# Performance work log

Measured on AMD Instinct MI355X. Metric: run time of the kernel, lower is better.

Reference implementation:

```python
import jax, jax.numpy as jnp
from jax import lax
import numpy as np

B = 4096          # batch
EMBED = 32        # embed_dim
HEADS = 2
MEM_SIZE = 4096
MEM_DIM = 256
TOPK = 10
LN_EPS = 1e-5


def setup_inputs() -> dict:
    key = jax.random.key(0)
    ks = jax.random.split(key, 32)
    rn = lambda i, shape, s=0.05: (jax.random.normal(ks[i], shape) * s).astype(jnp.float32)
    return {
        'x': jax.random.normal(ks[0], (B, 1, 28, 28), dtype=jnp.float32),
        'patch_w': rn(1, (32, 1, 4, 4)), 'patch_b': rn(2, (32,)),
        'blk_ln1_g': jnp.ones((2, 32), jnp.float32), 'blk_ln1_b': jnp.zeros((2, 32), jnp.float32),
        'blk_inproj_w': rn(3, (2, 96, 32)), 'blk_inproj_b': rn(4, (2, 96)),
        'blk_outproj_w': rn(5, (2, 32, 32)), 'blk_outproj_b': rn(6, (2, 32)),
        'blk_ln2_g': jnp.ones((2, 32), jnp.float32), 'blk_ln2_b': jnp.zeros((2, 32), jnp.float32),
        'blk_ff1_w': rn(7, (2, 128, 32)), 'blk_ff1_b': rn(8, (2, 128)),
        'blk_ff2_w': rn(9, (2, 32, 128)), 'blk_ff2_b': rn(10, (2, 32)),
        'lat_w': rn(11, (256, 1568)), 'lat_b': rn(12, (256,)),
        'memory': jax.random.normal(ks[13], (MEM_SIZE, MEM_DIM), dtype=jnp.float32),
        'dec_w': rn(14, (3136, 256)), 'dec_b': rn(15, (3136,)),
        'upt1_w': rn(16, (64, 32, 4, 4)), 'upt1_b': rn(17, (32,)),
        'c1_w': rn(18, (32, 32, 3, 3)), 'c1_b': rn(19, (32,)),
        'upt2_w': rn(20, (32, 16, 4, 4)), 'upt2_b': rn(21, (16,)),
        'c2_w': rn(22, (8, 16, 3, 3)), 'c2_b': rn(23, (8,)),
        'c3_w': rn(24, (1, 8, 1, 1)), 'c3_b': rn(25, (1,)),
    }


def _ln(x, g, b):
    m = jnp.mean(x, -1, keepdims=True)
    v = jnp.mean((x - m) ** 2, -1, keepdims=True)
    return (x - m) / jnp.sqrt(v + LN_EPS) * g + b


def _conv2d(x, w, b, stride=1, pad=0):
    out = lax.conv_general_dilated(x, w, (stride, stride), ((pad, pad), (pad, pad)),
                                   dimension_numbers=('NCHW', 'OIHW', 'NCHW'))
    return out + b[None, :, None, None]


def _conv_transpose2d(x, w, b, stride, pad):
    # w in torch layout [in, out, kh, kw]; equivalent fractionally-strided conv
    w_f = jnp.flip(w, (2, 3)).transpose(1, 0, 2, 3)  # OIHW
    k = w.shape[2]
    p = k - 1 - pad
    out = lax.conv_general_dilated(x, w_f, (1, 1), ((p, p), (p, p)),
                                   lhs_dilation=(stride, stride),
                                   dimension_numbers=('NCHW', 'OIHW', 'NCHW'))
    return out + b[None, :, None, None]


def _mha(x, wi, bi, wo, bo):
    Bn, S, D = x.shape
    Dh = D // HEADS
    qkv = x @ wi.T + bi                                  # [B,S,3D]
    q, k, v = jnp.split(qkv, 3, axis=-1)
    sp = lambda t: t.reshape(Bn, S, HEADS, Dh).transpose(0, 2, 1, 3)
    q, k, v = sp(q), sp(k), sp(v)
    scores = jnp.einsum('bhqd,bhkd->bhqk', q, k) / jnp.sqrt(jnp.asarray(Dh, x.dtype))
    att = jax.nn.softmax(scores, axis=-1)
    o = jnp.einsum('bhqk,bhkd->bhqd', att, v).transpose(0, 2, 1, 3).reshape(Bn, S, D)
    return o @ wo.T + bo


def _memory_read(latent, memory):
    # cosine-sim topk softmax-weighted gather (F.normalize eps=1e-12)
    mn = memory / jnp.clip(jnp.linalg.norm(memory, axis=1, keepdims=True), 1e-12)
    xn = latent / jnp.clip(jnp.linalg.norm(latent, axis=1, keepdims=True), 1e-12)
    sim = xn @ mn.T                                       # [B, MEM_SIZE]
    topk_sim, topk_idx = lax.top_k(sim, TOPK)
    w = jax.nn.softmax(topk_sim, axis=1)                  # [B, TOPK]
    sel = memory[topk_idx]                                # [B, TOPK, MEM_DIM]
    return jnp.einsum('bk,bkd->bd', w, sel)


def _forward(x, patch_w, patch_b, blk_ln1_g, blk_ln1_b, blk_inproj_w, blk_inproj_b,
             blk_outproj_w, blk_outproj_b, blk_ln2_g, blk_ln2_b, blk_ff1_w, blk_ff1_b,
             blk_ff2_w, blk_ff2_b, lat_w, lat_b, memory, dec_w, dec_b,
             upt1_w, upt1_b, c1_w, c1_b, upt2_w, upt2_b, c2_w, c2_b, c3_w, c3_b):
    Bn = x.shape[0]
    h = _conv2d(x, patch_w, patch_b, stride=4)            # [B,32,7,7]
    t = h.reshape(Bn, EMBED, 49).transpose(0, 2, 1)       # [B,49,32]
    for i in range(2):                                    # two SwinBlocks
        t = t + _mha(_ln(t, blk_ln1_g[i], blk_ln1_b[i]),
                     blk_inproj_w[i], blk_inproj_b[i], blk_outproj_w[i], blk_outproj_b[i])
        f = _ln(t, blk_ln2_g[i], blk_ln2_b[i])
        f = jax.nn.gelu(f @ blk_ff1_w[i].T + blk_ff1_b[i], approximate=False)
        t = t + (f @ blk_ff2_w[i].T + blk_ff2_b[i])
    latent = t.reshape(Bn, -1) @ lat_w.T + lat_b          # [B,256]
    mem_latent = _memory_read(latent, memory)             # [B,256]
    d = (mem_latent @ dec_w.T + dec_b).reshape(Bn, 64, 7, 7)  # dropout=eval identity
    d = jax.nn.relu(_conv_transpose2d(d, upt1_w, upt1_b, 2, 1))   # [B,32,14,14]
    d = jax.nn.relu(_conv2d(d, c1_w, c1_b, 1, 1))
    d = jax.nn.relu(_conv_transpose2d(d, upt2_w, upt2_b, 2, 1))   # [B,16,28,28]
    d = jax.nn.relu(_conv2d(d, c2_w, c2_b, 1, 1))                 # [B,8,28,28]
    return _conv2d(d, c3_w, c3_b, 1, 0)                           # [B,1,28,28]


def reference(x, patch_w, patch_b, blk_ln1_g, blk_ln1_b, blk_inproj_w, blk_inproj_b,
              blk_outproj_w, blk_outproj_b, blk_ln2_g, blk_ln2_b, blk_ff1_w, blk_ff1_b,
              blk_ff2_w, blk_ff2_b, lat_w, lat_b, memory, dec_w, dec_b,
              upt1_w, upt1_b, c1_w, c1_b, upt2_w, upt2_b, c2_w, c2_b, c3_w, c3_b):
    return _forward(x, patch_w, patch_b, blk_ln1_g, blk_ln1_b, blk_inproj_w, blk_inproj_b,
                    blk_outproj_w, blk_outproj_b, blk_ln2_g, blk_ln2_b, blk_ff1_w, blk_ff1_b,
                    blk_ff2_w, blk_ff2_b, lat_w, lat_b, memory, dec_w, dec_b,
                    upt1_w, upt1_b, c1_w, c1_b, upt2_w, upt2_b, c2_w, c2_b, c3_w, c3_b)
```

## Files before the change

kernel.cpp:

```cpp
#include <hip/hip_runtime.h>
#include <math.h>

#define B_TOT 4096
#define CHUNK 4096

typedef _Float16 half_t;
typedef _Float16 h2 __attribute__((ext_vector_type(2)));
typedef _Float16 h8v __attribute__((ext_vector_type(8)));
typedef float f4v __attribute__((ext_vector_type(4)));

#if __has_builtin(__builtin_amdgcn_fdot2)
#define FDOT2(a, b, c) __builtin_amdgcn_fdot2((a), (b), (c), false)
#else
#define FDOT2(a, b, c) fmaf((float)(a)[1], (float)(b)[1], fmaf((float)(a)[0], (float)(b)[0], (c)))
#endif

#define KSTR 36
#define VSTR 34
#define KBYTES (49 * 72)
#define WAVE_LDS (49 * 72 + 49 * 136)
#define WI_OFF  (4 * WAVE_LDS)
#define BLOCK_LDS (WI_OFF + 12288)

__global__ __launch_bounds__(256) void k_tokens(
    const float* __restrict__ x, const float* __restrict__ pw, const float* __restrict__ pb,
    const float* __restrict__ ln1g, const float* __restrict__ ln1b,
    const float* __restrict__ wi, const float* __restrict__ bi,
    const float* __restrict__ wo, const float* __restrict__ bo,
    const float* __restrict__ ln2g, const float* __restrict__ ln2b,
    const float* __restrict__ w1, const float* __restrict__ fb1,
    const float* __restrict__ w2t, const float* __restrict__ fb2,
    float* __restrict__ tokens)
{
    __shared__ __align__(16) unsigned char Lraw[BLOCK_LDS];
    const int tid = threadIdx.x;
    const int wv = tid >> 6, lane = tid & 63;
    const int b = blockIdx.x * 4 + wv;
    half_t* Kb = (half_t*)(Lraw + wv * WAVE_LDS);
    float*  Vb = (float*)(Lraw + wv * WAVE_LDS + KBYTES);
    const float* wiL = (const float*)(Lraw + WI_OFF);
    float* Lf = (float*)Lraw;
    const bool is_tok = lane < 49;
    const int s = is_tok ? lane : 48;
    const int py = s / 7, px = s % 7;

    {
        const float4* srcw = (const float4*)(wi);
        float4* dstw = (float4*)(Lraw + WI_OFF);
        for (int e = tid; e < 768; e += 256) dstw[e] = srcw[e];
    }

    float xv[16];
    const float* xb = x + (size_t)b * 784 + py * 112 + px * 4;
    #pragma unroll
    for (int r = 0; r < 4; ++r) {
        float4 vq = *(const float4*)(xb + r * 28);
        xv[4 * r + 0] = vq.x; xv[4 * r + 1] = vq.y;
        xv[4 * r + 2] = vq.z; xv[4 * r + 3] = vq.w;
    }
    float t[32];
    #pragma unroll 4
    for (int c = 0; c < 32; ++c) {
        float a = pb[c];
        const float* wr = pw + c * 16;
        #pragma unroll
        for (int i = 0; i < 16; ++i) a = fmaf(xv[i], wr[i], a);
        t[c] = a;
    }

    for (int blk = 0; blk < 2; ++blk) {
        const float* bib = bi + blk * 96;

        float mu = 0.f;
        #pragma unroll
        for (int c = 0; c < 32; ++c) mu += t[c];
        mu *= 0.03125f;
        float var = 0.f;
        #pragma unroll
        for (int c = 0; c < 32; ++c) { float d = t[c] - mu; var = fmaf(d, d, var); }
        float rstd = rsqrtf(var * 0.03125f + 1e-5f);
        float xn[32];
        #pragma unroll
        for (int c = 0; c < 32; ++c)
            xn[c] = (t[c] - mu) * rstd * ln1g[blk * 32 + c] + ln1b[blk * 32 + c];

        __syncthreads();

        #pragma unroll 4
        for (int d = 0; d < 32; ++d) {
            const float* wr = wiL + (32 + d) * 32;
            float a0 = bib[32 + d], a1 = 0.f;
            #pragma unroll
            for (int c2 = 0; c2 < 4; ++c2) {
                float4 wq = *(const float4*)&wr[4 * c2];
                a0 = fmaf(xn[4 * c2],     wq.x, a0);
                a0 = fmaf(xn[4 * c2 + 1], wq.y, a0);
                a0 = fmaf(xn[4 * c2 + 2], wq.z, a0);
                a0 = fmaf(xn[4 * c2 + 3], wq.w, a0);
            }
            #pragma unroll
            for (int c2 = 4; c2 < 8; ++c2) {
                float4 wq = *(const float4*)&wr[4 * c2];
                a1 = fmaf(xn[4 * c2],     wq.x, a1);
                a1 = fmaf(xn[4 * c2 + 1], wq.y, a1);
                a1 = fmaf(xn[4 * c2 + 2], wq.z, a1);
                a1 = fmaf(xn[4 * c2 + 3], wq.w, a1);
            }
            if (is_tok) Kb[s * KSTR + d] = (half_t)(a0 + a1);
        }
        #pragma unroll 4
        for (int d = 0; d < 32; ++d) {
            const float* wr = wiL + (64 + d) * 32;
            float a0 = bib[64 + d], a1 = 0.f;
            #pragma unroll
            for (int c2 = 0; c2 < 4; ++c2) {
                float4 wq = *(const float4*)&wr[4 * c2];
                a0 = fmaf(xn[4 * c2],     wq.x, a0);
                a0 = fmaf(xn[4 * c2 + 1], wq.y, a0);
                a0 = fmaf(xn[4 * c2 + 2], wq.z, a0);
                a0 = fmaf(xn[4 * c2 + 3], wq.w, a0);
            }
            #pragma unroll
            for (int c2 = 4; c2 < 8; ++c2) {
                float4 wq = *(const float4*)&wr[4 * c2];
                a1 = fmaf(xn[4 * c2],     wq.x, a1);
                a1 = fmaf(xn[4 * c2 + 1], wq.y, a1);
                a1 = fmaf(xn[4 * c2 + 2], wq.z, a1);
                a1 = fmaf(xn[4 * c2 + 3], wq.w, a1);
            }
            if (is_tok) Vb[s * VSTR + d] = a0 + a1;
        }
        float q0[32];
        #pragma unroll 4
        for (int d = 0; d < 32; ++d) {
            const float* wr = wiL + d * 32;
            float a0 = bib[d], a1 = 0.f;
            #pragma unroll
            for (int c2 = 0; c2 < 4; ++c2) {
                float4 wq = *(const float4*)&wr[4 * c2];
                a0 = fmaf(xn[4 * c2],     wq.x, a0);
                a0 = fmaf(xn[4 * c2 + 1], wq.y, a0);
                a0 = fmaf(xn[4 * c2 + 2], wq.z, a0);
                a0 = fmaf(xn[4 * c2 + 3], wq.w, a0);
            }
            #pragma unroll
            for (int c2 = 4; c2 < 8; ++c2) {
                float4 wq = *(const float4*)&wr[4 * c2];
                a1 = fmaf(xn[4 * c2],     wq.x, a1);
                a1 = fmaf(xn[4 * c2 + 1], wq.y, a1);
                a1 = fmaf(xn[4 * c2 + 2], wq.z, a1);
                a1 = fmaf(xn[4 * c2 + 3], wq.w, a1);
            }
            q0[d] = (a0 + a1) * 0.25f;
        }
        h2 qh[16];
        #pragma unroll
        for (int i = 0; i < 16; ++i) {
            h2 hh; hh[0] = (half_t)q0[2 * i]; hh[1] = (half_t)q0[2 * i + 1];
            qh[i] = hh;
        }

        __asm__ volatile("s_waitcnt lgkmcnt(0)" ::: "memory");

        float o[32];
        #pragma unroll
        for (int d = 0; d < 32; ++d) o[d] = 0.f;
        float l0 = 0.f, l1 = 0.f;
        union H4 { double qd; h2 p[2]; };
        for (int j = 0; j < 49; ++j) {
            const double* kr = (const double*)(Kb + j * KSTR);
            const float* vr = Vb + j * VSTR;
            H4 u0, u1, u2, u3, w0, w1h, w2h, w3;
            u0.qd = kr[0]; u1.qd = kr[1]; u2.qd = kr[2]; u3.qd = kr[3];
            w0.qd = kr[4]; w1h.qd = kr[5]; w2h.qd = kr[6]; w3.qd = kr[7];
            float s0a = 0.f, s0b = 0.f, s1a = 0.f, s1b = 0.f;
            s0a = FDOT2(u0.p[0], qh[0], s0a); s0a = FDOT2(u0.p[1], qh[1], s0a);
            s0b = FDOT2(u1.p[0], qh[2], s0b); s0b = FDOT2(u1.p[1], qh[3], s0b);
            s0a = FDOT2(u2.p[0], qh[4], s0a); s0a = FDOT2(u2.p[1], qh[5], s0a);
            s0b = FDOT2(u3.p[0], qh[6], s0b); s0b = FDOT2(u3.p[1], qh[7], s0b);
            s1a = FDOT2(w0.p[0], qh[8], s1a); s1a = FDOT2(w0.p[1], qh[9], s1a);
            s1b = FDOT2(w1h.p[0], qh[10], s1b); s1b = FDOT2(w1h.p[1], qh[11], s1b);
            s1a = FDOT2(w2h.p[0], qh[12], s1a); s1a = FDOT2(w2h.p[1], qh[13], s1a);
            s1b = FDOT2(w3.p[0], qh[14], s1b); s1b = FDOT2(w3.p[1], qh[15], s1b);
            float p0 = __expf(s0a + s0b), p1 = __expf(s1a + s1b);
            l0 += p0; l1 += p1;
            #pragma unroll
            for (int i = 0; i < 8; ++i) {
                float2 va = *(const float2*)&vr[2 * i];
                o[2 * i]     = fmaf(p0, va.x, o[2 * i]);
                o[2 * i + 1] = fmaf(p0, va.y, o[2 * i + 1]);
                float2 vc = *(const float2*)&vr[16 + 2 * i];
                o[16 + 2 * i]     = fmaf(p1, vc.x, o[16 + 2 * i]);
                o[16 + 2 * i + 1] = fmaf(p1, vc.y, o[16 + 2 * i + 1]);
            }
        }
        float il0 = 1.f / l0, il1 = 1.f / l1;
        #pragma unroll
        for (int d = 0; d < 16; ++d) { o[d] *= il0; o[16 + d] *= il1; }

        #pragma unroll
        for (int c = 0; c < 32; ++c) {
            const float* wr = wo + blk * 1024 + c * 32;
            float a = bo[blk * 32 + c];
            #pragma unroll
            for (int k2 = 0; k2 < 32; ++k2) a = fmaf(o[k2], wr[k2], a);
            t[c] += a;
        }

        mu = 0.f;
        #pragma unroll
        for (int c = 0; c < 32; ++c) mu += t[c];
        mu *= 0.03125f;
        var = 0.f;
        #pragma unroll
        for (int c = 0; c < 32; ++c) { float d = t[c] - mu; var = fmaf(d, d, var); }
        rstd = rsqrtf(var * 0.03125f + 1e-5f);
        #pragma unroll
        for (int c = 0; c < 32; ++c)
            xn[c] = (t[c] - mu) * rstd * ln2g[blk * 32 + c] + ln2b[blk * 32 + c];

        __syncthreads();

        {
            const float4* src1 = (const float4*)(w1 + blk * 4096);
            const float4* src2 = (const float4*)(w2t + blk * 4096);
            float4* dst = (float4*)Lraw;
            for (int e = tid; e < 1024; e += 256) dst[e] = src1[e];
            for (int e = tid; e < 1024; e += 256) dst[1024 + e] = src2[e];
            if (blk == 0) {
                const float4* srcw = (const float4*)(wi + 3072);
                float4* dstw = (float4*)(Lraw + WI_OFF);
                for (int e = tid; e < 768; e += 256) dstw[e] = srcw[e];
            }
        }
        __syncthreads();

        const float* w2L = Lf + 4096;
        #pragma unroll 2
        for (int j = 0; j < 128; ++j) {
            const float* wr = Lf + j * 32;
            float ha = fb1[blk * 128 + j], hb = 0.f;
            #pragma unroll
            for (int c2 = 0; c2 < 4; ++c2) {
                float4 wq = *(const float4*)&wr[4 * c2];
                ha = fmaf(xn[4 * c2],     wq.x, ha);
                ha = fmaf(xn[4 * c2 + 1], wq.y, ha);
                ha = fmaf(xn[4 * c2 + 2], wq.z, ha);
                ha = fmaf(xn[4 * c2 + 3], wq.w, ha);
            }
            #pragma unroll
            for (int c2 = 4; c2 < 8; ++c2) {
                float4 wq = *(const float4*)&wr[4 * c2];
                hb = fmaf(xn[4 * c2],     wq.x, hb);
                hb = fmaf(xn[4 * c2 + 1], wq.y, hb);
                hb = fmaf(xn[4 * c2 + 2], wq.z, hb);
                hb = fmaf(xn[4 * c2 + 3], wq.w, hb);
            }
            float h = ha + hb;
            h = 0.5f * h * (1.f + erff(h * 0.7071067811865476f));
            const float* w2r = w2L + j * 32;
            #pragma unroll
            for (int c2 = 0; c2 < 8; ++c2) {
                float4 wq = *(const float4*)&w2r[4 * c2];
                t[4 * c2]     = fmaf(h, wq.x, t[4 * c2]);
                t[4 * c2 + 1] = fmaf(h, wq.y, t[4 * c2 + 1]);
                t[4 * c2 + 2] = fmaf(h, wq.z, t[4 * c2 + 2]);
                t[4 * c2 + 3] = fmaf(h, wq.w, t[4 * c2 + 3]);
            }
        }
        #pragma unroll
        for (int c = 0; c < 32; ++c) t[c] += fb2[blk * 32 + c];
    }

    if (is_tok) {
        float* op = tokens + (size_t)b * 1568 + s * 32;
        #pragma unroll
        for (int c = 0; c < 32; c += 4) {
            float4 vv = make_float4(t[c], t[c + 1], t[c + 2], t[c + 3]);
            *(float4*)&op[c] = vv;
        }
    }
}

__global__ __launch_bounds__(256) void k_gemm(
    const float* __restrict__ A, const float* __restrict__ Bm,
    const float* __restrict__ bias, float* __restrict__ C,
    int M, int N, int K, int relu)
{
    __shared__ float As[16 * 132];
    __shared__ float Bs[16 * 68];
    const int n0 = blockIdx.x * 64, m0 = blockIdx.y * 128;
    const int tid = threadIdx.x;
    const int tx = tid & 15, ty = tid >> 4;
    const int lr = tid >> 1, lk = (tid & 1) * 8;
    const int br = tid >> 2, bk = (tid & 3) * 4;
    float acc[8][4] = {{0.f}};
    for (int k0 = 0; k0 < K; k0 += 16) {
        float4 av0 = *(const float4*)&A[(size_t)(m0 + lr) * K + k0 + lk];
        float4 av1 = *(const float4*)&A[(size_t)(m0 + lr) * K + k0 + lk + 4];
        float4 bv0 = *(const float4*)&Bm[(size_t)(n0 + br) * K + k0 + bk];
        As[(lk + 0) * 132 + lr] = av0.x;
        As[(lk + 1) * 132 + lr] = av0.y;
        As[(lk + 2) * 132 + lr] = av0.z;
        As[(lk + 3) * 132 + lr] = av0.w;
        As[(lk + 4) * 132 + lr] = av1.x;
        As[(lk + 5) * 132 + lr] = av1.y;
        As[(lk + 6) * 132 + lr] = av1.z;
        As[(lk + 7) * 132 + lr] = av1.w;
        Bs[(bk + 0) * 68 + br] = bv0.x;
        Bs[(bk + 1) * 68 + br] = bv0.y;
        Bs[(bk + 2) * 68 + br] = bv0.z;
        Bs[(bk + 3) * 68 + br] = bv0.w;
        __syncthreads();
        #pragma unroll
        for (int k = 0; k < 16; ++k) {
            float4 a0 = *(const float4*)&As[k * 132 + ty * 8];
            float4 a1 = *(const float4*)&As[k * 132 + ty * 8 + 4];
            float4 bv = *(const float4*)&Bs[k * 68 + tx * 4];
            float a8[8] = {a0.x, a0.y, a0.z, a0.w, a1.x, a1.y, a1.z, a1.w};
            float b4[4] = {bv.x, bv.y, bv.z, bv.w};
            #pragma unroll
            for (int i = 0; i < 8; ++i)
                #pragma unroll
                for (int j = 0; j < 4; ++j)
                    acc[i][j] = fmaf(a8[i], b4[j], acc[i][j]);
        }
        __syncthreads();
    }
    #pragma unroll
    for (int i = 0; i < 8; ++i) {
        int m = m0 + ty * 8 + i;
        #pragma unroll
        for (int j = 0; j < 4; ++j) {
            int n = n0 + tx * 4 + j;
            float v = acc[i][j] + (bias ? bias[n] : 0.f);
            if (relu) v = fmaxf(v, 0.f);
            C[(size_t)m * N + n] = v;
        }
    }
}

__global__ __launch_bounds__(256) void k_sgemm(
    const float* __restrict__ A, const float* __restrict__ Bm,
    float* __restrict__ C, int M, int N, int K)
{
    __shared__ __align__(16) half_t Ah[64 * 40];
    __shared__ __align__(16) half_t Al[64 * 40];
    __shared__ __align__(16) half_t Bh[128 * 40];
    __shared__ __align__(16) half_t Bl[128 * 40];
    const int tid = threadIdx.x;
    const int n0 = blockIdx.x * 128, m0 = blockIdx.y * 64;
    const int w = tid >> 6, lane = tid & 63;
    const int wm = (w >> 1) * 32, wn = (w & 1) * 64;
    const int lr = lane & 15, lk = lane >> 4;

    const int ar = tid >> 2, aseg = (tid & 3) * 8;
    const int br = tid >> 1, bseg = (tid & 1) * 16;

    f4v acch[2][4], accm[2][4];
    #pragma unroll
    for (int i = 0; i < 2; ++i)
        #pragma unroll
        for (int j = 0; j < 4; ++j) {
            acch[i][j] = (f4v){0.f, 0.f, 0.f, 0.f};
            accm[i][j] = (f4v){0.f, 0.f, 0.f, 0.f};
        }

    for (int k0 = 0; k0 < K; k0 += 32) {
        {
            const float* ap = A + (size_t)(m0 + ar) * K + k0 + aseg;
            float4 a0 = *(const float4*)ap;
            float4 a1 = *(const float4*)(ap + 4);
            float av[8] = {a0.x, a0.y, a0.z, a0.w, a1.x, a1.y, a1.z, a1.w};
            h8v ah, al;
            #pragma unroll
            for (int i = 0; i < 8; ++i) {
                half_t h = (half_t)av[i];
                ah[i] = h;
                al[i] = (half_t)((av[i] - (float)h) * 2048.0f);
            }
            *(h8v*)&Ah[ar * 40 + aseg] = ah;
            *(h8v*)&Al[ar * 40 + aseg] = al;

            const float* bp = Bm + (size_t)(n0 + br) * K + k0 + bseg;
            float4 b0 = *(const float4*)bp;
            float4 b1 = *(const float4*)(bp + 4);
            float4 b2 = *(const float4*)(bp + 8);
            float4 b3 = *(const float4*)(bp + 12);
            float bv[16] = {b0.x, b0.y, b0.z, b0.w, b1.x, b1.y, b1.z, b1.w,
                            b2.x, b2.y, b2.z, b2.w, b3.x, b3.y, b3.z, b3.w};
            h8v bh0, bh1, bl0, bl1;
            #pragma unroll
            for (int i = 0; i < 8; ++i) {
                half_t h = (half_t)bv[i];
                bh0[i] = h;
                bl0[i] = (half_t)((bv[i] - (float)h) * 2048.0f);
                half_t h2v = (half_t)bv[8 + i];
                bh1[i] = h2v;
                bl1[i] = (half_t)((bv[8 + i] - (float)h2v) * 2048.0f);
            }
            *(h8v*)&Bh[br * 40 + bseg]     = bh0;
            *(h8v*)&Bh[br * 40 + bseg + 8] = bh1;
            *(h8v*)&Bl[br * 40 + bseg]     = bl0;
            *(h8v*)&Bl[br * 40 + bseg + 8] = bl1;
        }
        __syncthreads();
        h8v afh[2], afl[2], bfh[4], bfl[4];
        #pragma unroll
        for (int i = 0; i < 2; ++i) {
            afh[i] = *(const h8v*)&Ah[(wm + i * 16 + lr) * 40 + lk * 8];
            afl[i] = *(const h8v*)&Al[(wm + i * 16 + lr) * 40 + lk * 8];
        }
        #pragma unroll
        for (int j = 0; j < 4; ++j) {
            bfh[j] = *(const h8v*)&Bh[(wn + j * 16 + lr) * 40 + lk * 8];
            bfl[j] = *(const h8v*)&Bl[(wn + j * 16 + lr) * 40 + lk * 8];
        }
        #pragma unroll
        for (int i = 0; i < 2; ++i)
            #pragma unroll
            for (int j = 0; j < 4; ++j) {
                acch[i][j] = __builtin_amdgcn_mfma_f32_16x16x32_f16(afh[i], bfh[j], acch[i][j], 0, 0, 0);
                accm[i][j] = __builtin_amdgcn_mfma_f32_16x16x32_f16(afh[i], bfl[j], accm[i][j], 0, 0, 0);
                accm[i][j] = __builtin_amdgcn_mfma_f32_16x16x32_f16(afl[i], bfh[j], accm[i][j], 0, 0, 0);
            }
        __syncthreads();
    }

    #pragma unroll
    for (int j = 0; j < 4; ++j) {
        int n = n0 + wn + j * 16 + lr;
        #pragma unroll
        for (int i = 0; i < 2; ++i) {
            #pragma unroll
            for (int r = 0; r < 4; ++r) {
                int m = m0 + wm + i * 16 + lk * 4 + r;
                C[(size_t)m * N + n] = acch[i][j][r] + accm[i][j][r] * (1.0f / 2048.0f);
            }
        }
    }
}

__global__ __launch_bounds__(256) void k_dgemm(
    const float* __restrict__ A, const float* __restrict__ Bm,
    const float* __restrict__ bias, half_t* __restrict__ C,
    int M, int N, int K)
{
    __shared__ __align__(16) half_t As[64 * 40];
    __shared__ __align__(16) half_t Bs[128 * 40];
    const int tid = threadIdx.x;
    const int n0 = blockIdx.x * 128, m0 = blockIdx.y * 64;
    const int w = tid >> 6, lane = tid & 63;
    const int wm = (w >> 1) * 32, wn = (w & 1) * 64;
    const int lr = lane & 15, lk = lane >> 4;

    const int ar = tid >> 2, aseg = (tid & 3) * 8;
    const int br = tid >> 1, bseg = (tid & 1) * 16;

    f4v acc[2][4];
    #pragma unroll
    for (int i = 0; i < 2; ++i)
        #pragma unroll
        for (int j = 0; j < 4; ++j) acc[i][j] = (f4v){0.f, 0.f, 0.f, 0.f};

    for (int k0 = 0; k0 < K; k0 += 32) {
        {
            const float* ap = A + (size_t)(m0 + ar) * K + k0 + aseg;
            float4 a0 = *(const float4*)ap;
            float4 a1 = *(const float4*)(ap + 4);
            h8v ha;
            ha[0] = (half_t)a0.x; ha[1] = (half_t)a0.y;
            ha[2] = (half_t)a0.z; ha[3] = (half_t)a0.w;
            ha[4] = (half_t)a1.x; ha[5] = (half_t)a1.y;
            ha[6] = (half_t)a1.z; ha[7] = (half_t)a1.w;
            *(h8v*)&As[ar * 40 + aseg] = ha;

            const float* bp = Bm + (size_t)(n0 + br) * K + k0 + bseg;
            float4 b0 = *(const float4*)bp;
            float4 b1 = *(const float4*)(bp + 4);
            float4 b2 = *(const float4*)(bp + 8);
            float4 b3 = *(const float4*)(bp + 12);
            h8v hb0, hb1;
            hb0[0] = (half_t)b0.x; hb0[1] = (half_t)b0.y;
            hb0[2] = (half_t)b0.z; hb0[3] = (half_t)b0.w;
            hb0[4] = (half_t)b1.x; hb0[5] = (half_t)b1.y;
            hb0[6] = (half_t)b1.z; hb0[7] = (half_t)b1.w;
            hb1[0] = (half_t)b2.x; hb1[1] = (half_t)b2.y;
            hb1[2] = (half_t)b2.z; hb1[3] = (half_t)b2.w;
            hb1[4] = (half_t)b3.x; hb1[5] = (half_t)b3.y;
            hb1[6] = (half_t)b3.z; hb1[7] = (half_t)b3.w;
            *(h8v*)&Bs[br * 40 + bseg] = hb0;
            *(h8v*)&Bs[br * 40 + bseg + 8] = hb1;
        }
        __syncthreads();
        h8v af[2], bfr[4];
        #pragma unroll
        for (int i = 0; i < 2; ++i)
            af[i] = *(const h8v*)&As[(wm + i * 16 + lr) * 40 + lk * 8];
        #pragma unroll
        for (int j = 0; j < 4; ++j)
            bfr[j] = *(const h8v*)&Bs[(wn + j * 16 + lr) * 40 + lk * 8];
        #pragma unroll
        for (int i = 0; i < 2; ++i)
            #pragma unroll
            for (int j = 0; j < 4; ++j)
                acc[i][j] = __builtin_amdgcn_mfma_f32_16x16x32_f16(af[i], bfr[j], acc[i][j], 0, 0, 0);
        __syncthreads();
    }

    #pragma unroll
    for (int j = 0; j < 4; ++j) {
        int n = n0 + wn + j * 16 + lr;
        float bv = bias[n];
        #pragma unroll
        for (int i = 0; i < 2; ++i) {
            #pragma unroll
            for (int r = 0; r < 4; ++r) {
                int m = m0 + wm + i * 16 + lk * 4 + r;
                C[(size_t)m * N + n] = (half_t)fmaxf(acc[i][j][r] + bv, 0.f);
            }
        }
    }
}

__global__ __launch_bounds__(256) void k_fuse(
    const float* __restrict__ wt1, const float* __restrict__ upt1_b,
    const float* __restrict__ dec_w, const float* __restrict__ dec_b,
    float* __restrict__ Wf, float* __restrict__ bf)
{
    __shared__ float WL[4][64][32];
    const int p = blockIdx.x;
    const int k = threadIdx.x;
    const int y = p / 14, x = p % 14;

    int ky0 = 0, iy0 = 0, ky1 = 0, iy1 = 0, nky = 0;
    for (int ky = 0; ky < 4; ++ky) {
        int iyn = y + 1 - ky;
        if (iyn < 0 || (iyn & 1)) continue;
        int iy = iyn >> 1;
        if (iy > 6) continue;
        if (nky == 0) { ky0 = ky; iy0 = iy; } else { ky1 = ky; iy1 = iy; }
        ++nky;
    }
    int kx0 = 0, ix0 = 0, kx1 = 0, ix1 = 0, nkx = 0;
    for (int kx = 0; kx < 4; ++kx) {
        int ixn = x + 1 - kx;
        if (ixn < 0 || (ixn & 1)) continue;
        int ix = ixn >> 1;
        if (ix > 6) continue;
        if (nkx == 0) { kx0 = kx; ix0 = ix; } else { kx1 = kx; ix1 = ix; }
        ++nkx;
    }
    const int ntap = nky * nkx;

    for (int e = k; e < ntap * 2048; e += 256) {
        int t = e >> 11, c = (e >> 5) & 63, o = e & 31;
        int ti = (nkx == 2) ? (t >> 1) : t;
        int tj = (nkx == 2) ? (t & 1) : 0;
        int ky = ti ? ky1 : ky0;
        int kx = tj ? kx1 : kx0;
        WL[t][c][o] = wt1[((c * 32 + o) * 4 + ky) * 4 + kx];
    }
    __syncthreads();

    float acc[32];
    #pragma unroll
    for (int o = 0; o < 32; ++o) acc[o] = 0.f;
    float bacc = 0.f;

    for (int t = 0; t < ntap; ++t) {
        int ti = (nkx == 2) ? (t >> 1) : t;
        int tj = (nkx == 2) ? (t & 1) : 0;
        int iy = ti ? iy1 : iy0;
        int ix = tj ? ix1 : ix0;
        int rbase = iy * 7 + ix;
        for (int c = 0; c < 64; ++c) {
            int row = c * 49 + rbase;
            float v = dec_w[(size_t)row * 256 + k];
            const float* wr = &WL[t][c][0];
            #pragma unroll
            for (int o8 = 0; o8 < 8; ++o8) {
                float4 wq = *(const float4*)&wr[4 * o8];
                acc[4 * o8 + 0] = fmaf(wq.x, v, acc[4 * o8 + 0]);
                acc[4 * o8 + 1] = fmaf(wq.y, v, acc[4 * o8 + 1]);
                acc[4 * o8 + 2] = fmaf(wq.z, v, acc[4 * o8 + 2]);
                acc[4 * o8 + 3] = fmaf(wq.w, v, acc[4 * o8 + 3]);
            }
            if (k < 32) bacc = fmaf(WL[t][c][k], dec_b[row], bacc);
        }
    }
// ... 203 lines not shown

    const int oc = lane & 15;
    const int kseg = (lane >> 4) * 8;

    f4v res[13];
    #pragma unroll
    for (int j = 0; j < 13; ++j) {
        const int job = w + 4 * j;
        const int q = job / 13, tile = job - q * 13;
        const int py = q >> 1, px = q & 1;
        int p = tile * 16 + (lane & 15);
        if (p > 195) p = 195;
        const int ty = p / 14, tx = p % 14;
        f4v a = (f4v){0.f, 0.f, 0.f, 0.f};
        #pragma unroll
        for (int t = 0; t < 4; ++t) {
            const int wy = t >> 1, wx = t & 1;
            h8v bf = *(const h8v*)&pk3h[((size_t)((q * 4 + t) * 16 + oc)) * 32 + kseg];
            h8v af = *(const h8v*)&Pin[((ty + py + wy) * 16 + (tx + px + wx)) * 40 + kseg];
            a = __builtin_amdgcn_mfma_f32_16x16x32_f16(af, bf, a, 0, 0, 0);
        }
        res[j] = a;
    }
    __syncthreads();

    const bool active2 = tid < 196;
    int row = active2 ? tid / 7 : 0;
    int tx0b = active2 ? (tid % 7) * 4 : 0;
    const float bco = bt2[oc];

    float acc2[4][8];
    #pragma unroll
    for (int i = 0; i < 4; ++i)
        #pragma unroll
        for (int o = 0; o < 8; ++o) acc2[i][o] = 0.f;

    #pragma unroll
    for (int g = 0; g < 2; ++g) {
        for (int e = tid; e < 7680; e += 256) P2[e] = 0.f;
        __syncthreads();
        if ((oc >> 3) == g) {
            #pragma unroll
            for (int j = 0; j < 13; ++j) {
                const int job = w + 4 * j;
                const int q = job / 13, tile = job - q * 13;
                const int py = q >> 1, px = q & 1;
                const int pr0 = tile * 16 + (lane >> 4) * 4;
                #pragma unroll
                for (int r = 0; r < 4; ++r) {
                    int p = pr0 + r;
                    if (p < 196) {
                        int Y = 2 * (p / 14) + py, X = 2 * (p % 14) + px;
                        P2[((oc & 7) * 30 + Y + 1) * 32 + (X + 1)] = fmaxf(res[j][r] + bco, 0.f);
                    }
                }
            }
        }
        __syncthreads();
        for (int cl = 0; cl < 8; ++cl) {
            const float* Pb = &P2[(cl * 30 + row) * 32 + tx0b];
            const float* wb = pk4 + (size_t)(g * 8 + cl) * 72;
            #pragma unroll
            for (int ky = 0; ky < 3; ++ky) {
                float4 a = *(const float4*)&Pb[ky * 32];
                float4 bq = *(const float4*)&Pb[ky * 32 + 4];
                float rowb[8] = {a.x, a.y, a.z, a.w, bq.x, bq.y, bq.z, bq.w};
                #pragma unroll
                for (int kx = 0; kx < 3; ++kx) {
                    const float* wt = wb + (ky * 3 + kx) * 8;
                    #pragma unroll
                    for (int o = 0; o < 8; ++o) {
                        float wv2 = wt[o];
                        #pragma unroll
                        for (int i = 0; i < 4; ++i)
                            acc2[i][o] = fmaf(rowb[i + kx], wv2, acc2[i][o]);
                    }
                }
            }
        }
        __syncthreads();
    }

    if (active2) {
        const float bias3 = b3[0];
        #pragma unroll
        for (int i = 0; i < 4; ++i) {
            float r = bias3;
            #pragma unroll
            for (int o = 0; o < 8; ++o) r += fmaxf(acc2[i][o] + b2[o], 0.f) * w3[o];
            out[(size_t)b * 784 + row * 28 + tx0b + i] = r;
        }
    }
}

extern "C" void kernel_launch(void* const* d_in, const int* in_sizes, int n_in,
                              void* d_out, int out_size, void* d_ws, size_t ws_size,
                              hipStream_t stream)
{
    const float* x       = (const float*)d_in[0];
    const float* patch_w = (const float*)d_in[1];
    const float* patch_b = (const float*)d_in[2];
    const float* ln1g    = (const float*)d_in[3];
    const float* ln1b    = (const float*)d_in[4];
    const float* wi      = (const float*)d_in[5];
    const float* bi      = (const float*)d_in[6];
    const float* wo      = (const float*)d_in[7];
    const float* bo      = (const float*)d_in[8];
    const float* ln2g    = (const float*)d_in[9];
    const float* ln2b    = (const float*)d_in[10];
    const float* w1      = (const float*)d_in[11];
    const float* b1      = (const float*)d_in[12];
    const float* w2      = (const float*)d_in[13];
    const float* b2      = (const float*)d_in[14];
    const float* lat_w   = (const float*)d_in[15];
    const float* lat_b   = (const float*)d_in[16];
    const float* memory  = (const float*)d_in[17];
    const float* dec_w   = (const float*)d_in[18];
    const float* dec_b   = (const float*)d_in[19];
    const float* upt1_w  = (const float*)d_in[20];
    const float* upt1_b  = (const float*)d_in[21];
    const float* c1_w    = (const float*)d_in[22];
    const float* c1_b    = (const float*)d_in[23];
    const float* upt2_w  = (const float*)d_in[24];
    const float* upt2_b  = (const float*)d_in[25];
    const float* c2_w    = (const float*)d_in[26];
    const float* c2_b    = (const float*)d_in[27];
    const float* c3_w    = (const float*)d_in[28];
    const float* c3_b    = (const float*)d_in[29];
    float* outp = (float*)d_out;

    float* ws = (float*)d_ws;
    size_t off = 0;
    auto alloc = [&](size_t n) { float* p = ws + off; off += (n + 63) & ~(size_t)63; return p; };
    float* tokens     = alloc((size_t)B_TOT * 1568);
    float* latent     = alloc((size_t)B_TOT * 256);
    float* dots       = alloc((size_t)B_TOT * 4096);
    float* mem_latent = alloc((size_t)B_TOT * 256);
    float* inv_mn     = alloc(4096);
    half_t* pk2h      = (half_t*)alloc(4608);
    half_t* pk3h      = (half_t*)alloc(4096);
    float* pk4        = alloc(1152);
    float* pk5        = alloc(8192);
    float* Wf         = alloc((size_t)6272 * 256);
    float* bf         = alloc(6272);
    half_t* d1h       = (half_t*)alloc((size_t)CHUNK * 6272 / 2);
    half_t* d2h       = (half_t*)alloc((size_t)CHUNK * 6272 / 2);
    (void)in_sizes; (void)n_in; (void)out_size; (void)ws_size;

    k_pack<<<36, 256, 0, stream>>>(c1_w, upt2_w, c2_w, w2, pk2h, pk3h, pk4, pk5);
    k_fuse<<<196, 256, 0, stream>>>(upt1_w, upt1_b, dec_w, dec_b, Wf, bf);

    k_tokens<<<B_TOT / 4, 256, 0, stream>>>(x, patch_w, patch_b, ln1g, ln1b, wi, bi,
                                            wo, bo, ln2g, ln2b, w1, b1, pk5, b2, tokens);
    k_gemm<<<dim3(256 / 64, B_TOT / 128), 256, 0, stream>>>(tokens, lat_w, lat_b, latent,
                                                            B_TOT, 256, 1568, 0);
    k_mnorm<<<4096, 256, 0, stream>>>(memory, inv_mn);
    k_sgemm<<<dim3(4096 / 128, B_TOT / 64), 256, 0, stream>>>(latent, memory, dots,
                                                              B_TOT, 4096, 256);
    k_memread<<<B_TOT, 256, 0, stream>>>(latent, dots, inv_mn, memory, mem_latent);

    for (int c = 0; c < B_TOT / CHUNK; ++c) {
        const float* ml = mem_latent + (size_t)c * CHUNK * 256;
        k_dgemm<<<dim3(6272 / 128, CHUNK / 64), 256, 0, stream>>>(ml, Wf, bf, d1h,
                                                                  CHUNK, 6272, 256);
        k_conv1  <<<CHUNK / 2, 256, 0, stream>>>(d1h, pk2h, c1_b, d2h);
        k_convt23<<<CHUNK, 256, 0, stream>>>(d2h, pk3h, upt2_b, pk4, c2_b, c3_w, c3_b,
                                             outp + (size_t)c * CHUNK * 784);
    }
}
```

Before: 1.144 ms.

## Route latent projection through split-fp16 MFMA GEMM and pack token math as float2

The latent projection (4096x1568 by 256) moves from a scalar fp32 SIMT GEMM to the existing split-precision fp16 MFMA GEMM kernel, which gains an optional bias argument. The separate scalar GEMM kernel is removed. Separately, the per-token transformer kernel is rewritten to use two-wide float vectors so the compiler can emit packed FMA instructions for the LayerNorm, projection, attention and MLP arithmetic. Risks are small numeric differences from the hi/lo fp16 split on the K=1568 reduction and from the changed summation order.

```diff
diff --git a/kernel.cpp b/kernel.cpp
--- a/kernel.cpp
+++ b/kernel.cpp
@@ -8,6 +8,7 @@
 typedef _Float16 h2 __attribute__((ext_vector_type(2)));
 typedef _Float16 h8v __attribute__((ext_vector_type(8)));
 typedef float f4v __attribute__((ext_vector_type(4)));
+typedef float f2v __attribute__((ext_vector_type(2)));
 
 #if __has_builtin(__builtin_amdgcn_fdot2)
 #define FDOT2(a, b, c) __builtin_amdgcn_fdot2((a), (b), (c), false)
@@ -50,108 +51,97 @@
         for (int e = tid; e < 768; e += 256) dstw[e] = srcw[e];
     }
 
-    float xv[16];
+    f2v xv2[8];
     const float* xb = x + (size_t)b * 784 + py * 112 + px * 4;
     #pragma unroll
     for (int r = 0; r < 4; ++r) {
         float4 vq = *(const float4*)(xb + r * 28);
-        xv[4 * r + 0] = vq.x; xv[4 * r + 1] = vq.y;
-        xv[4 * r + 2] = vq.z; xv[4 * r + 3] = vq.w;
-    }
-    float t[32];
-    #pragma unroll 4
+        f2v lo; lo[0] = vq.x; lo[1] = vq.y;
+        f2v hi; hi[0] = vq.z; hi[1] = vq.w;
+        xv2[2 * r] = lo; xv2[2 * r + 1] = hi;
+    }
+    f2v t2[16];
+    #pragma unroll
     for (int c = 0; c < 32; ++c) {
-        float a = pb[c];
         const float* wr = pw + c * 16;
-        #pragma unroll
-        for (int i = 0; i < 16; ++i) a = fmaf(xv[i], wr[i], a);
-        t[c] = a;
+        f2v a2 = (f2v){0.f, 0.f};
+        #pragma unroll
+        for (int c2 = 0; c2 < 4; ++c2) {
+            float4 wq = *(const float4*)&wr[4 * c2];
+            f2v w0; w0[0] = wq.x; w0[1] = wq.y;
+            f2v w1v; w1v[0] = wq.z; w1v[1] = wq.w;
+            a2 += xv2[2 * c2] * w0;
+            a2 += xv2[2 * c2 + 1] * w1v;
+        }
+        t2[c >> 1][c & 1] = pb[c] + a2[0] + a2[1];
     }
 
     for (int blk = 0; blk < 2; ++blk) {
         const float* bib = bi + blk * 96;
 
-        float mu = 0.f;
-        #pragma unroll
-        for (int c = 0; c < 32; ++c) mu += t[c];
-        mu *= 0.03125f;
-        float var = 0.f;
-        #pragma unroll
-        for (int c = 0; c < 32; ++c) { float d = t[c] - mu; var = fmaf(d, d, var); }
-        float rstd = rsqrtf(var * 0.03125f + 1e-5f);
-        float xn[32];
-        #pragma unroll
-        for (int c = 0; c < 32; ++c)
-            xn[c] = (t[c] - mu) * rstd * ln1g[blk * 32 + c] + ln1b[blk * 32 + c];
+        f2v mu2 = (f2v){0.f, 0.f};
+        #pragma unroll
+        for (int i = 0; i < 16; ++i) mu2 += t2[i];
+        float mu = (mu2[0] + mu2[1]) * 0.03125f;
+        f2v mub; mub[0] = mu; mub[1] = mu;
+        f2v var2 = (f2v){0.f, 0.f};
+        #pragma unroll
+        for (int i = 0; i < 16; ++i) { f2v d = t2[i] - mub; var2 += d * d; }
+        float rstd = rsqrtf((var2[0] + var2[1]) * 0.03125f + 1e-5f);
+        f2v rstd2; rstd2[0] = rstd; rstd2[1] = rstd;
+        f2v xn2[16];
+        {
+            const f2v* g2 = (const f2v*)(ln1g + blk * 32);
+            const f2v* bl2 = (const f2v*)(ln1b + blk * 32);
+            #pragma unroll
+            for (int i = 0; i < 16; ++i)
+                xn2[i] = (t2[i] - mub) * rstd2 * g2[i] + bl2[i];
+        }
 
         __syncthreads();
 
         #pragma unroll 4
         for (int d = 0; d < 32; ++d) {
             const float* wr = wiL + (32 + d) * 32;
-            float a0 = bib[32 + d], a1 = 0.f;
-            #pragma unroll
-            for (int c2 = 0; c2 < 4; ++c2) {
+            f2v a2 = (f2v){0.f, 0.f};
+            #pragma unroll
+            for (int c2 = 0; c2 < 8; ++c2) {
                 float4 wq = *(const float4*)&wr[4 * c2];
-                a0 = fmaf(xn[4 * c2],     wq.x, a0);
-                a0 = fmaf(xn[4 * c2 + 1], wq.y, a0);
-                a0 = fmaf(xn[4 * c2 + 2], wq.z, a0);
-                a0 = fmaf(xn[4 * c2 + 3], wq.w, a0);
-            }
-            #pragma unroll
-            for (int c2 = 4; c2 < 8; ++c2) {
-                float4 wq = *(const float4*)&wr[4 * c2];
-                a1 = fmaf(xn[4 * c2],     wq.x, a1);
-                a1 = fmaf(xn[4 * c2 + 1], wq.y, a1);
-                a1 = fmaf(xn[4 * c2 + 2], wq.z, a1);
-                a1 = fmaf(xn[4 * c2 + 3], wq.w, a1);
-            }
-            if (is_tok) Kb[s * KSTR + d] = (half_t)(a0 + a1);
+                f2v w0; w0[0] = wq.x; w0[1] = wq.y;
+                f2v w1v; w1v[0] = wq.z; w1v[1] = wq.w;
+                a2 += xn2[2 * c2] * w0;
+                a2 += xn2[2 * c2 + 1] * w1v;
+            }
+            if (is_tok) Kb[s * KSTR + d] = (half_t)(bib[32 + d] + a2[0] + a2[1]);
         }
         #pragma unroll 4
         for (int d = 0; d < 32; ++d) {
             const float* wr = wiL + (64 + d) * 32;
-            float a0 = bib[64 + d], a1 = 0.f;
-            #pragma unroll
-            for (int c2 = 0; c2 < 4; ++c2) {
+            f2v a2 = (f2v){0.f, 0.f};
+            #pragma unroll
+            for (int c2 = 0; c2 < 8; ++c2) {
                 float4 wq = *(const float4*)&wr[4 * c2];
-                a0 = fmaf(xn[4 * c2],     wq.x, a0);
-                a0 = fmaf(xn[4 * c2 + 1], wq.y, a0);
-                a0 = fmaf(xn[4 * c2 + 2], wq.z, a0);
-                a0 = fmaf(xn[4 * c2 + 3], wq.w, a0);
-            }
-            #pragma unroll
-            for (int c2 = 4; c2 < 8; ++c2) {
-                float4 wq = *(const float4*)&wr[4 * c2];
-                a1 = fmaf(xn[4 * c2],     wq.x, a1);
-                a1 = fmaf(xn[4 * c2 + 1], wq.y, a1);
-                a1 = fmaf(xn[4 * c2 + 2], wq.z, a1);
-                a1 = fmaf(xn[4 * c2 + 3], wq.w, a1);
-            }
-            if (is_tok) Vb[s * VSTR + d] = a0 + a1;
+                f2v w0; w0[0] = wq.x; w0[1] = wq.y;
+                f2v w1v; w1v[0] = wq.z; w1v[1] = wq.w;
+                a2 += xn2[2 * c2] * w0;
+                a2 += xn2[2 * c2 + 1] * w1v;
+            }
+            if (is_tok) Vb[s * VSTR + d] = bib[64 + d] + a2[0] + a2[1];
         }
         float q0[32];
         #pragma unroll 4
         for (int d = 0; d < 32; ++d) {
             const float* wr = wiL + d * 32;
-            float a0 = bib[d], a1 = 0.f;
-            #pragma unroll
-            for (int c2 = 0; c2 < 4; ++c2) {
+            f2v a2 = (f2v){0.f, 0.f};
+            #pragma unroll
+            for (int c2 = 0; c2 < 8; ++c2) {
                 float4 wq = *(const float4*)&wr[4 * c2];
-                a0 = fmaf(xn[4 * c2],     wq.x, a0);
-                a0 = fmaf(xn[4 * c2 + 1], wq.y, a0);
-                a0 = fmaf(xn[4 * c2 + 2], wq.z, a0);
-                a0 = fmaf(xn[4 * c2 + 3], wq.w, a0);
-            }
-            #pragma unroll
-            for (int c2 = 4; c2 < 8; ++c2) {
-                float4 wq = *(const float4*)&wr[4 * c2];
-                a1 = fmaf(xn[4 * c2],     wq.x, a1);
-                a1 = fmaf(xn[4 * c2 + 1], wq.y, a1);
-                a1 = fmaf(xn[4 * c2 + 2], wq.z, a1);
-                a1 = fmaf(xn[4 * c2 + 3], wq.w, a1);
-            }
-            q0[d] = (a0 + a1) * 0.25f;
+                f2v w0; w0[0] = wq.x; w0[1] = wq.y;
+                f2v w1v; w1v[0] = wq.z; w1v[1] = wq.w;
+                a2 += xn2[2 * c2] * w0;
+                a2 += xn2[2 * c2 + 1] * w1v;
+            }
+            q0[d] = (bib[d] + a2[0] + a2[1]) * 0.25f;
         }
         h2 qh[16];
         #pragma unroll
@@ -162,9 +152,9 @@
 
         __asm__ volatile("s_waitcnt lgkmcnt(0)" ::: "memory");
 
-        float o[32];
-        #pragma unroll
-        for (int d = 0; d < 32; ++d) o[d] = 0.f;
+        f2v o2[16];
+        #pragma unroll
+        for (int i = 0; i < 16; ++i) o2[i] = (f2v){0.f, 0.f};
         float l0 = 0.f, l1 = 0.f;
         union H4 { double qd; h2 p[2]; };
         for (int j = 0; j < 49; ++j) {
@@ -184,40 +174,56 @@
             s1b = FDOT2(w3.p[0], qh[14], s1b); s1b = FDOT2(w3.p[1], qh[15], s1b);
             float p0 = __expf(s0a + s0b), p1 = __expf(s1a + s1b);
             l0 += p0; l1 += p1;
+            f2v p02; p02[0] = p0; p02[1] = p0;
+            f2v p12; p12[0] = p1; p12[1] = p1;
             #pragma unroll
             for (int i = 0; i < 8; ++i) {
-                float2 va = *(const float2*)&vr[2 * i];
-                o[2 * i]     = fmaf(p0, va.x, o[2 * i]);
-                o[2 * i + 1] = fmaf(p0, va.y, o[2 * i + 1]);
-                float2 vc = *(const float2*)&vr[16 + 2 * i];
-                o[16 + 2 * i]     = fmaf(p1, vc.x, o[16 + 2 * i]);
-                o[16 + 2 * i + 1] = fmaf(p1, vc.y, o[16 + 2 * i + 1]);
-            }
-        }
-        float il0 = 1.f / l0, il1 = 1.f / l1;
-        #pragma unroll
-        for (int d = 0; d < 16; ++d) { o[d] *= il0; o[16 + d] *= il1; }
+                f2v va = *(const f2v*)&vr[2 * i];
+                o2[i] += p02 * va;
+                f2v vc = *(const f2v*)&vr[16 + 2 * i];
+                o2[8 + i] += p12 * vc;
+            }
+        }
+        {
+            float il0 = 1.f / l0, il1 = 1.f / l1;
+            f2v il02; il02[0] = il0; il02[1] = il0;
+            f2v il12; il12[0] = il1; il12[1] = il1;
+            #pragma unroll
+            for (int i = 0; i < 8; ++i) { o2[i] *= il02; o2[8 + i] *= il12; }
+        }
 
         #pragma unroll
         for (int c = 0; c < 32; ++c) {
             const float* wr = wo + blk * 1024 + c * 32;
-            float a = bo[blk * 32 + c];
-            #pragma unroll
-            for (int k2 = 0; k2 < 32; ++k2) a = fmaf(o[k2], wr[k2], a);
-            t[c] += a;
-        }
-
-        mu = 0.f;
-        #pragma unroll
-        for (int c = 0; c < 32; ++c) mu += t[c];
-        mu *= 0.03125f;
-        var = 0.f;
-        #pragma unroll
-        for (int c = 0; c < 32; ++c) { float d = t[c] - mu; var = fmaf(d, d, var); }
-        rstd = rsqrtf(var * 0.03125f + 1e-5f);
-        #pragma unroll
-        for (int c = 0; c < 32; ++c)
-            xn[c] = (t[c] - mu) * rstd * ln2g[blk * 32 + c] + ln2b[blk * 32 + c];
+            f2v a2 = (f2v){0.f, 0.f};
+            #pragma unroll
+            for (int c2 = 0; c2 < 8; ++c2) {
+                float4 wq = *(const float4*)&wr[4 * c2];
+                f2v w0; w0[0] = wq.x; w0[1] = wq.y;
+                f2v w1v; w1v[0] = wq.z; w1v[1] = wq.w;
+                a2 += o2[2 * c2] * w0;
+                a2 += o2[2 * c2 + 1] * w1v;
+            }
+            t2[c >> 1][c & 1] += bo[blk * 32 + c] + a2[0] + a2[1];
+        }
+
+        mu2 = (f2v){0.f, 0.f};
+        #pragma unroll
+        for (int i = 0; i < 16; ++i) mu2 += t2[i];
+        mu = (mu2[0] + mu2[1]) * 0.03125f;
+        mub[0] = mu; mub[1] = mu;
+        var2 = (f2v){0.f, 0.f};
+        #pragma unroll
+        for (int i = 0; i < 16; ++i) { f2v d = t2[i] - mub; var2 += d * d; }
+        rstd = rsqrtf((var2[0] + var2[1]) * 0.03125f + 1e-5f);
+        rstd2[0] = rstd; rstd2[1] = rstd;
+        {
+            const f2v* g2 = (const f2v*)(ln2g + blk * 32);
+            const f2v* bl2 = (const f2v*)(ln2b + blk * 32);
+            #pragma unroll
+            for (int i = 0; i < 16; ++i)
+                xn2[i] = (t2[i] - mub) * rstd2 * g2[i] + bl2[i];
+        }
 
         __syncthreads();
 
@@ -239,110 +245,50 @@
         #pragma unroll 2
         for (int j = 0; j < 128; ++j) {
             const float* wr = Lf + j * 32;
-            float ha = fb1[blk * 128 + j], hb = 0.f;
-            #pragma unroll
-            for (int c2 = 0; c2 < 4; ++c2) {
+            f2v h2a = (f2v){0.f, 0.f};
+            #pragma unroll
+            for (int c2 = 0; c2 < 8; ++c2) {
                 float4 wq = *(const float4*)&wr[4 * c2];
-                ha = fmaf(xn[4 * c2],     wq.x, ha);
-                ha = fmaf(xn[4 * c2 + 1], wq.y, ha);
-                ha = fmaf(xn[4 * c2 + 2], wq.z, ha);
-                ha = fmaf(xn[4 * c2 + 3], wq.w, ha);
-            }
-            #pragma unroll
-            for (int c2 = 4; c2 < 8; ++c2) {
-                float4 wq = *(const float4*)&wr[4 * c2];
-                hb = fmaf(xn[4 * c2],     wq.x, hb);
-                hb = fmaf(xn[4 * c2 + 1], wq.y, hb);
-                hb = fmaf(xn[4 * c2 + 2], wq.z, hb);
-                hb = fmaf(xn[4 * c2 + 3], wq.w, hb);
-            }
-            float h = ha + hb;
+                f2v w0; w0[0] = wq.x; w0[1] = wq.y;
+                f2v w1v; w1v[0] = wq.z; w1v[1] = wq.w;
+                h2a += xn2[2 * c2] * w0;
+                h2a += xn2[2 * c2 + 1] * w1v;
+            }
+            float h = fb1[blk * 128 + j] + h2a[0] + h2a[1];
             h = 0.5f * h * (1.f + erff(h * 0.7071067811865476f));
+            f2v hh; hh[0] = h; hh[1] = h;
             const float* w2r = w2L + j * 32;
             #pragma unroll
             for (int c2 = 0; c2 < 8; ++c2) {
                 float4 wq = *(const float4*)&w2r[4 * c2];
-                t[4 * c2]     = fmaf(h, wq.x, t[4 * c2]);
-                t[4 * c2 + 1] = fmaf(h, wq.y, t[4 * c2 + 1]);
-                t[4 * c2 + 2] = fmaf(h, wq.z, t[4 * c2 + 2]);
-                t[4 * c2 + 3] = fmaf(h, wq.w, t[4 * c2 + 3]);
-            }
-        }
-        #pragma unroll
-        for (int c = 0; c < 32; ++c) t[c] += fb2[blk * 32 + c];
+                f2v w0; w0[0] = wq.x; w0[1] = wq.y;
+                f2v w1v; w1v[0] = wq.z; w1v[1] = wq.w;
+                t2[2 * c2]     += hh * w0;
+                t2[2 * c2 + 1] += hh * w1v;
+            }
+        }
+        {
+            const f2v* fb22 = (const f2v*)(fb2 + blk * 32);
+            #pragma unroll
+            for (int i = 0; i < 16; ++i) t2[i] += fb22[i];
+        }
     }
 
     if (is_tok) {
         float* op = tokens + (size_t)b * 1568 + s * 32;
         #pragma unroll
-        for (int c = 0; c < 32; c += 4) {
-            float4 vv = make_float4(t[c], t[c + 1], t[c + 2], t[c + 3]);
-            *(float4*)&op[c] = vv;
+        for (int i = 0; i < 8; ++i) {
+            float4 vv = make_float4(t2[2 * i][0], t2[2 * i][1],
+                                    t2[2 * i + 1][0], t2[2 * i + 1][1]);
+            *(float4*)&op[4 * i] = vv;
         }
     }
 }
 
-__global__ __launch_bounds__(256) void k_gemm(
+__global__ __launch_bounds__(256) void k_sgemm(
     const float* __restrict__ A, const float* __restrict__ Bm,
     const float* __restrict__ bias, float* __restrict__ C,
-    int M, int N, int K, int relu)
-{
-    __shared__ float As[16 * 132];
-    __shared__ float Bs[16 * 68];
-    const int n0 = blockIdx.x * 64, m0 = blockIdx.y * 128;
-    const int tid = threadIdx.x;
-    const int tx = tid & 15, ty = tid >> 4;
-    const int lr = tid >> 1, lk = (tid & 1) * 8;
-    const int br = tid >> 2, bk = (tid & 3) * 4;
-    float acc[8][4] = {{0.f}};
-    for (int k0 = 0; k0 < K; k0 += 16) {
-        float4 av0 = *(const float4*)&A[(size_t)(m0 + lr) * K + k0 + lk];
-        float4 av1 = *(const float4*)&A[(size_t)(m0 + lr) * K + k0 + lk + 4];
-        float4 bv0 = *(const float4*)&Bm[(size_t)(n0 + br) * K + k0 + bk];
-        As[(lk + 0) * 132 + lr] = av0.x;
-        As[(lk + 1) * 132 + lr] = av0.y;
-        As[(lk + 2) * 132 + lr] = av0.z;
-        As[(lk + 3) * 132 + lr] = av0.w;
-        As[(lk + 4) * 132 + lr] = av1.x;
-        As[(lk + 5) * 132 + lr] = av1.y;
-        As[(lk + 6) * 132 + lr] = av1.z;
-        As[(lk + 7) * 132 + lr] = av1.w;
-        Bs[(bk + 0) * 68 + br] = bv0.x;
-        Bs[(bk + 1) * 68 + br] = bv0.y;
-        Bs[(bk + 2) * 68 + br] = bv0.z;
-        Bs[(bk + 3) * 68 + br] = bv0.w;
-        __syncthreads();
-        #pragma unroll
-        for (int k = 0; k < 16; ++k) {
-            float4 a0 = *(const float4*)&As[k * 132 + ty * 8];
-            float4 a1 = *(const float4*)&As[k * 132 + ty * 8 + 4];
-            float4 bv = *(const float4*)&Bs[k * 68 + tx * 4];
-            float a8[8] = {a0.x, a0.y, a0.z, a0.w, a1.x, a1.y, a1.z, a1.w};
-            float b4[4] = {bv.x, bv.y, bv.z, bv.w};
-            #pragma unroll
-            for (int i = 0; i < 8; ++i)
-                #pragma unroll
-                for (int j = 0; j < 4; ++j)
-                    acc[i][j] = fmaf(a8[i], b4[j], acc[i][j]);
-        }
-        __syncthreads();
-    }
-    #pragma unroll
-    for (int i = 0; i < 8; ++i) {
-        int m = m0 + ty * 8 + i;
-        #pragma unroll
-        for (int j = 0; j < 4; ++j) {
-            int n = n0 + tx * 4 + j;
-            float v = acc[i][j] + (bias ? bias[n] : 0.f);
-            if (relu) v = fmaxf(v, 0.f);
-            C[(size_t)m * N + n] = v;
-        }
-    }
-}
-
-__global__ __launch_bounds__(256) void k_sgemm(
-    const float* __restrict__ A, const float* __restrict__ Bm,
-    float* __restrict__ C, int M, int N, int K)
+    int M, int N, int K)
 {
     __shared__ __align__(16) half_t Ah[64 * 40];
     __shared__ __align__(16) half_t Al[64 * 40];
@@ -395,9 +341,9 @@
                 half_t h = (half_t)bv[i];
                 bh0[i] = h;
                 bl0[i] = (half_t)((bv[i] - (float)h) * 2048.0f);
-                half_t h2v = (half_t)bv[8 + i];
-                bh1[i] = h2v;
-                bl1[i] = (half_t)((bv[8 + i] - (float)h2v) * 2048.0f);
+                half_t hq = (half_t)bv[8 + i];
+                bh1[i] = hq;
+                bl1[i] = (half_t)((bv[8 + i] - (float)hq) * 2048.0f);
             }
             *(h8v*)&Bh[br * 40 + bseg]     = bh0;
             *(h8v*)&Bh[br * 40 + bseg + 8] = bh1;
@@ -430,12 +376,13 @@
     #pragma unroll
     for (int j = 0; j < 4; ++j) {
         int n = n0 + wn + j * 16 + lr;
+        float bv = bias ? bias[n] : 0.f;
         #pragma unroll
         for (int i = 0; i < 2; ++i) {
             #pragma unroll
             for (int r = 0; r < 4; ++r) {
                 int m = m0 + wm + i * 16 + lk * 4 + r;
-                C[(size_t)m * N + n] = acch[i][j][r] + accm[i][j][r] * (1.0f / 2048.0f);
+                C[(size_t)m * N + n] = acch[i][j][r] + accm[i][j][r] * (1.0f / 2048.0f) + bv;
             }
         }
     }
@@ -945,10 +892,10 @@
 
     k_tokens<<<B_TOT / 4, 256, 0, stream>>>(x, patch_w, patch_b, ln1g, ln1b, wi, bi,
                                             wo, bo, ln2g, ln2b, w1, b1, pk5, b2, tokens);
-    k_gemm<<<dim3(256 / 64, B_TOT / 128), 256, 0, stream>>>(tokens, lat_w, lat_b, latent,
-                                                            B_TOT, 256, 1568, 0);
+    k_sgemm<<<dim3(256 / 128, B_TOT / 64), 256, 0, stream>>>(tokens, lat_w, lat_b, latent,
+                                                             B_TOT, 256, 1568);
     k_mnorm<<<4096, 256, 0, stream>>>(memory, inv_mn);
-    k_sgemm<<<dim3(4096 / 128, B_TOT / 64), 256, 0, stream>>>(latent, memory, dots,
+    k_sgemm<<<dim3(4096 / 128, B_TOT / 64), 256, 0, stream>>>(latent, memory, nullptr, dots,
                                                               B_TOT, 4096, 256);
     k_memread<<<B_TOT, 256, 0, stream>>>(latent, dots, inv_mn, memory, mem_latent);
 
```

Result: faster. 1.065 ms (-6.9%).
